# Kernel optimization log

Measured on AMD Instinct MI355X. Metric: run time of the kernel, lower is better.

The kernel has to match this reference:

```python
import jax, jax.numpy as jnp
import numpy as np

HID, H, LAT, R = 2048, 16, 512, 32
DH = HID // H          # 128 head_dim
C = DH - R             # 96 content_dim
B, S = 2, 2048


def rotate_half(x):
    h = x.shape[-1] // 2
    return jnp.concatenate([-x[..., h:], x[..., :h]], axis=-1)


def rope_tables(seq_len, dim):
    inv_freq = 1.0 / (10000.0 ** (jnp.arange(0, dim, 2, dtype=jnp.float32) / dim))
    t = jnp.arange(seq_len, dtype=jnp.float32)
    freqs = t[:, None] * inv_freq[None, :]          # [S, dim/2]
    emb = jnp.concatenate([freqs, freqs], axis=-1)  # [S, dim]
    return jnp.cos(emb), jnp.sin(emb)


def setup_inputs() -> dict:
    key = jax.random.key(0)
    ks = jax.random.split(key, 11)
    def lin(k, out_dim, in_dim):
        return jax.random.normal(k, (out_dim, in_dim), jnp.float32) / np.sqrt(in_dim)
    return {
        "x": jax.random.normal(ks[0], (B, S, HID), jnp.float32),
        "Wq_down": lin(ks[1], LAT, HID),
        "Wq_up": lin(ks[2], C * H, LAT),
        "Wq_rope": lin(ks[3], R * H, LAT),
        "Wkv_down": lin(ks[4], LAT, HID),
        "Wk_up": lin(ks[5], C * H, LAT),
        "Wk_rope": lin(ks[6], R, HID),
        "Wv_up": lin(ks[7], HID, LAT),
        "Wo": lin(ks[8], HID, HID),
        "bo": jnp.zeros((HID,), jnp.float32),
    }


def reference(x, Wq_down, Wq_up, Wq_rope, Wkv_down, Wk_up, Wk_rope, Wv_up, Wo, bo):
    Bs, Sl, _ = x.shape
    cos, sin = rope_tables(Sl, R)                       # [S, R]
    cos_b = cos[None, :, None, :]                       # [1,S,1,R]
    sin_b = sin[None, :, None, :]

    # low-rank Q path
    q_lat = jnp.einsum('bsh,lh->bsl', x, Wq_down)       # [B,S,LAT]
    q_c = jnp.einsum('bsl,cl->bsc', q_lat, Wq_up).reshape(Bs, Sl, H, C)
    q_r = jnp.einsum('bsl,rl->bsr', q_lat, Wq_rope).reshape(Bs, Sl, H, R)
    q_r = q_r * cos_b + rotate_half(q_r) * sin_b

    # low-rank KV path
    kv_lat = jnp.einsum('bsh,lh->bsl', x, Wkv_down)     # [B,S,LAT]
    k_c = jnp.einsum('bsl,cl->bsc', kv_lat, Wk_up).reshape(Bs, Sl, H, C)
    k_r = jnp.einsum('bsh,rh->bsr', x, Wk_rope)[:, :, None, :]   # [B,S,1,R]
    k_r = k_r * cos_b + rotate_half(k_r) * sin_b        # [B,S,1,R] (shared per head)
    k_r = jnp.broadcast_to(k_r, (Bs, Sl, H, R))
    v = jnp.einsum('bsl,dl->bsd', kv_lat, Wv_up).reshape(Bs, Sl, H, DH)

    q = jnp.concatenate([q_c, q_r], axis=-1)            # [B,S,H,DH]
    k = jnp.concatenate([k_c, k_r], axis=-1)

    scores = jnp.einsum('bqhd,bkhd->bhqk', q, k) / np.sqrt(DH)
    causal = jnp.triu(jnp.ones((Sl, Sl), bool), k=1)
    scores = jnp.where(causal[None, None], -10000.0, scores)
    attn = jax.nn.softmax(scores, axis=-1)
    ctx = jnp.einsum('bhqk,bkhd->bqhd', attn, v).reshape(Bs, Sl, HID)
    return jnp.einsum('bsd,od->bso', ctx, Wo) + bo
```

## Files before the change

### kernel.cpp

```cpp
#include <hip/hip_runtime.h>
#include <math.h>

#define HIDN 2048
#define NH   16
#define LATN 512
#define RD   32
#define DHD  128
#define CDIM 96
#define NB   2
#define SEQ  2048
#define MTOT 4096

typedef __attribute__((ext_vector_type(8))) short bf8_t;
typedef __attribute__((ext_vector_type(4))) float f4_t;
typedef __attribute__((ext_vector_type(4))) short s4_t;

__device__ __forceinline__ short f2bf(float f) {
    union { float f; unsigned u; } x; x.f = f;
    unsigned r = x.u + 0x7fffu + ((x.u >> 16) & 1u);
    return (short)(r >> 16);
}
__device__ __forceinline__ float bf2f(short s) {
    union { float f; unsigned u; } x; x.u = ((unsigned)(unsigned short)s) << 16;
    return x.f;
}
__device__ __forceinline__ void gload16(const void* g, void* l) {
    __builtin_amdgcn_global_load_lds(
        (const __attribute__((address_space(1))) void*)g,
        (__attribute__((address_space(3))) void*)l, 16, 0, 0);
}

__global__ __launch_bounds__(256)
void cvt_all(const float* __restrict__ x,  const float* __restrict__ w0,
             const float* __restrict__ w1, const float* __restrict__ w2,
             const float* __restrict__ w3, const float* __restrict__ w4,
             const float* __restrict__ w5, const float* __restrict__ w6,
             const float* __restrict__ w7,
             short* xb, short* o0, short* o1, short* o2, short* o3,
             short* o4, short* o5, short* o6, short* o7)
{
    int bid = blockIdx.x;
    const float* src; short* dst; int rel;
    if      (bid < 4096) { src = x;  dst = xb; rel = bid; }
    else if (bid < 4608) { src = w0; dst = o0; rel = bid - 4096; }
    else if (bid < 4992) { src = w1; dst = o1; rel = bid - 4608; }
    else if (bid < 5120) { src = w2; dst = o2; rel = bid - 4992; }
    else if (bid < 5632) { src = w3; dst = o3; rel = bid - 5120; }
    else if (bid < 6016) { src = w4; dst = o4; rel = bid - 5632; }
    else if (bid < 6048) { src = w5; dst = o5; rel = bid - 6016; }
    else if (bid < 6560) { src = w6; dst = o6; rel = bid - 6048; }
    else                 { src = w7; dst = o7; rel = bid - 6560; }
    int base = rel * 2048 + threadIdx.x * 8;
    float4 a = *(const float4*)(src + base);
    float4 b = *(const float4*)(src + base + 4);
    s4_t r0 = { f2bf(a.x), f2bf(a.y), f2bf(a.z), f2bf(a.w) };
    s4_t r1 = { f2bf(b.x), f2bf(b.y), f2bf(b.z), f2bf(b.w) };
    *(s4_t*)(dst + base)     = r0;
    *(s4_t*)(dst + base + 4) = r1;
}

#define EPI_DOWN 0
#define EPI_UP   1
#define EPI_WO   2

template<int KTOT, int EPI>
__global__ __launch_bounds__(256)
void gemm_t(const short* __restrict__ A, const short* __restrict__ W,
            const short* __restrict__ W2,
            void* __restrict__ o1, void* __restrict__ o2,
            void* __restrict__ o3, void* __restrict__ o4,
            const float* __restrict__ bias)
{
    __shared__ short As[2][4096];
    __shared__ short Bs[2][4096];
    const int tid  = threadIdx.x;
    const int w    = tid >> 6;
    const int lane = tid & 63;
    const int l16  = lane & 15;
    const int quad = lane >> 4;
    const int m0 = blockIdx.x * 128;
    int n0 = blockIdx.y * 128;
    const int wm = (w & 1) * 64;
    const int wn = (w >> 1) * 64;

    const short* Ap = A;
    const short* Wp = W;
    int lda, Nrow, job = 0;
    if (EPI == EPI_DOWN) { lda = 2048; Nrow = 1056; }
    if (EPI == EPI_WO)   { lda = 2048; Nrow = 2048; }
    if (EPI == EPI_UP) {
        lda = 1024;
        if (blockIdx.y < 16) { Nrow = 2048; }
        else { job = 1; Ap = A + 512; Wp = W2; n0 = ((int)blockIdx.y - 16) * 128; Nrow = 3584; }
    }

    int srow[2], skc[2], ldso[2];
#pragma unroll
    for (int j = 0; j < 2; ++j) {
        int c = (w * 32 + j * 16) * 4 + lane;
        srow[j] = c >> 2;
        skc[j]  = (c & 3) ^ (srow[j] & 3);
        ldso[j] = (w * 32 + j * 16) * 32;
    }
    const int xq = quad ^ (l16 & 3);

    auto stage = [&](int k0, int buf) {
#pragma unroll
        for (int j = 0; j < 2; ++j) {
            const short* ga = Ap + (size_t)(m0 + srow[j]) * lda + k0 + skc[j] * 8;
            gload16(ga, &As[buf][ldso[j]]);
            int gn = n0 + srow[j]; if (gn >= Nrow) gn = Nrow - 1;
            const short* gb = Wp + (size_t)gn * KTOT + k0 + skc[j] * 8;
            gload16(gb, &Bs[buf][ldso[j]]);
        }
    };

    f4_t acc[4][4];
#pragma unroll
    for (int i = 0; i < 4; ++i)
#pragma unroll
        for (int j = 0; j < 4; ++j) acc[i][j] = (f4_t){0.f, 0.f, 0.f, 0.f};

    stage(0, 0);
    const int nk = KTOT / 32;
    for (int t = 0; t < nk; ++t) {
        const int cur = t & 1;
        __syncthreads();
        if (t + 1 < nk) stage((t + 1) * 32, cur ^ 1);
        bf8_t af[4], bfr[4];
#pragma unroll
        for (int i = 0; i < 4; ++i)
            af[i] = *(const bf8_t*)&As[cur][((wm + i * 16 + l16) * 4 + xq) * 8];
#pragma unroll
        for (int j = 0; j < 4; ++j)
            bfr[j] = *(const bf8_t*)&Bs[cur][((wn + j * 16 + l16) * 4 + xq) * 8];
#pragma unroll
        for (int i = 0; i < 4; ++i)
#pragma unroll
            for (int j = 0; j < 4; ++j)
                acc[i][j] = __builtin_amdgcn_mfma_f32_16x16x32_bf16(
                    af[i], bfr[j], acc[i][j], 0, 0, 0);
    }

#pragma unroll
    for (int mi = 0; mi < 4; ++mi) {
#pragma unroll
        for (int nj = 0; nj < 4; ++nj) {
            const int gm = m0 + wm + mi * 16 + quad * 4;
            const int gn = n0 + wn + nj * 16 + l16;
            const int bb = gm >> 11, ss = gm & 2047;
            if (EPI == EPI_DOWN) {
                if (n0 < 1024) {
                    short* o = (short*)o1 + (size_t)gm * 1024 + gn;
#pragma unroll
                    for (int r = 0; r < 4; ++r) o[(size_t)r * 1024] = f2bf(acc[mi][nj][r]);
                } else if (gn < 1056) {
                    short* o = (short*)o2 + (size_t)gm * 32 + (gn - 1024);
#pragma unroll
                    for (int r = 0; r < 4; ++r) o[(size_t)r * 32] = f2bf(acc[mi][nj][r]);
                }
            } else if (EPI == EPI_WO) {
                float* o = (float*)o1 + (size_t)gm * 2048 + gn;
                float bv = bias[gn];
#pragma unroll
                for (int r = 0; r < 4; ++r) o[(size_t)r * 2048] = acc[mi][nj][r] + bv;
            } else {
                if (job == 0) {
                    if (gn < 1536) {
                        int hh = gn / CDIM, cc = gn % CDIM;
                        short* o = (short*)o1 +
                            (((size_t)(bb * NH + hh) * SEQ + ss) * DHD + cc);
#pragma unroll
                        for (int r = 0; r < 4; ++r) o[(size_t)r * DHD] = f2bf(acc[mi][nj][r]);
                    } else {
                        short* o = (short*)o2 + (size_t)gm * 512 + (gn - 1536);
#pragma unroll
                        for (int r = 0; r < 4; ++r) o[(size_t)r * 512] = f2bf(acc[mi][nj][r]);
                    }
                } else {
                    if (gn < 1536) {
                        int hh = gn / CDIM, cc = gn % CDIM;
                        short* o = (short*)o3 +
                            (((size_t)(bb * NH + hh) * SEQ + ss) * DHD + cc);
#pragma unroll
                        for (int r = 0; r < 4; ++r) o[(size_t)r * DHD] = f2bf(acc[mi][nj][r]);
                    } else {
                        int n2 = gn - 1536;
                        int h2 = n2 >> 7, dh = n2 & 127;
                        size_t idx = ((size_t)(bb * NH + h2) * DHD + dh) * SEQ + ss;
                        s4_t pk = { f2bf(acc[mi][nj][0]), f2bf(acc[mi][nj][1]),
                                    f2bf(acc[mi][nj][2]), f2bf(acc[mi][nj][3]) };
                        *(s4_t*)((short*)o4 + idx) = pk;
                    }
                }
            }
        }
    }
}

__global__ void rope_q_kernel(const short* __restrict__ qr, short* __restrict__ qh)
{
    int idx = blockIdx.x * blockDim.x + threadIdx.x;
    int m = idx >> 9;
    int h = (idx >> 5) & 15;
    int r = idx & 31;
    int b = m >> 11, s = m & (SEQ - 1);
    float invf = expf(-((float)(2 * (r & 15)) / 32.0f) * 9.210340371976184f);
    float f = (float)s * invf;
    float cs = cosf(f), sn = sinf(f);
    float val = bf2f(qr[(size_t)m * 512 + h * 32 + r]);
    float partner = bf2f(qr[(size_t)m * 512 + h * 32 + (r ^ 16)]);
    float rot = (r < 16) ? -partner : partner;
    qh[((size_t)(b * NH + h) * SEQ + s) * DHD + CDIM + r] = f2bf(val * cs + rot * sn);
}

__global__ void rope_k_kernel(const short* __restrict__ kr, short* __restrict__ kh)
{
    int idx = blockIdx.x * blockDim.x + threadIdx.x;
    int m = idx >> 5;
    int r = idx & 31;
    int b = m >> 11, s = m & (SEQ - 1);
    float invf = expf(-((float)(2 * (r & 15)) / 32.0f) * 9.210340371976184f);
    float f = (float)s * invf;
    float cs = cosf(f), sn = sinf(f);
    float val = bf2f(kr[(size_t)m * 32 + r]);
    float partner = bf2f(kr[(size_t)m * 32 + (r ^ 16)]);
    float rot = (r < 16) ? -partner : partner;
    short o = f2bf(val * cs + rot * sn);
    short* dst = kh + ((size_t)b * NH * SEQ + s) * DHD + CDIM + r;
#pragma unroll
    for (int h = 0; h < NH; ++h) dst[(size_t)h * SEQ * DHD] = o;
}

__global__ __launch_bounds__(256)
void attn_mfma(const short* __restrict__ qh, const short* __restrict__ kh,
               const short* __restrict__ vt, short* __restrict__ ctx)
{
    const int h = blockIdx.y, b = blockIdx.z;
    __shared__ short Ks[2][4096];
    __shared__ short Vs[2][4096];
    __shared__ short Ps[4][16][40];
    const int tid  = threadIdx.x;
    const int w    = tid >> 6;
    const int lane = tid & 63;
    const int l16  = lane & 15;
    const int quad = lane >> 4;
    const float scale = 0.08838834764831845f;

    const short* khead = kh + (size_t)(b * NH + h) * SEQ * DHD;
    const short* vhead = vt + (size_t)(b * NH + h) * DHD * SEQ;

    int koff[2], voff[2], ldso[2];
#pragma unroll
    for (int j = 0; j < 2; ++j) {
        int s = j * 256 + tid;
        int key = s >> 4, dch = (s & 15) ^ (key & 15);
        koff[j] = key * DHD + dch * 8;
        int d = s >> 2, kc = (s & 3) ^ ((d >> 1) & 3);
        voff[j] = d * SEQ + kc * 8;
        ldso[j] = (j * 256 + w * 64) * 8;
    }

    for (int phase = 0; phase < 2; ++phase) {
        const int qb = phase ? (31 - (int)blockIdx.x) : (int)blockIdx.x;
        const int q0 = qb * 64;

        bf8_t qf[4];
        {
            const short* qp = qh + ((size_t)(b * NH + h) * SEQ + q0 + w * 16 + l16) * DHD
                                 + quad * 8;
#pragma unroll
            for (int ks = 0; ks < 4; ++ks) {
                bf8_t raw = *(const bf8_t*)(qp + ks * 32);
#pragma unroll
                for (int j = 0; j < 8; ++j) qf[ks][j] = f2bf(bf2f(raw[j]) * scale);
            }
        }

        f4_t O[8];
#pragma unroll
        for (int i = 0; i < 8; ++i) O[i] = (f4_t){0.f, 0.f, 0.f, 0.f};
        float m_run[4], l_run[4];
#pragma unroll
        for (int r = 0; r < 4; ++r) { m_run[r] = -3e38f; l_run[r] = 0.f; }

        const int ntiles = 2 * qb + 2;
        __syncthreads();
#pragma unroll
        for (int j = 0; j < 2; ++j) {
            gload16(khead + koff[j], &Ks[0][ldso[j]]);
            gload16(vhead + voff[j], &Vs[0][ldso[j]]);
        }

        for (int t = 0; t < ntiles; ++t) {
            const int cur = t & 1;
            const int c0 = t * 32;
            __syncthreads();
            if (t + 1 < ntiles) {
                const short* kt = khead + (size_t)(c0 + 32) * DHD;
#pragma unroll
                for (int j = 0; j < 2; ++j) {
                    gload16(kt + koff[j], &Ks[cur ^ 1][ldso[j]]);
                    gload16(vhead + voff[j] + c0 + 32, &Vs[cur ^ 1][ldso[j]]);
                }
            }

            f4_t S0 = {0.f, 0.f, 0.f, 0.f}, S1 = {0.f, 0.f, 0.f, 0.f};
#pragma unroll
            for (int ks = 0; ks < 4; ++ks) {
                int dch = ks * 4 + quad;
                int si0 = l16 * 16 + (dch ^ l16);
                int si1 = (l16 + 16) * 16 + (dch ^ l16);
                bf8_t b0 = *(const bf8_t*)&Ks[cur][si0 * 8];
                bf8_t b1 = *(const bf8_t*)&Ks[cur][si1 * 8];
                S0 = __builtin_amdgcn_mfma_f32_16x16x32_bf16(qf[ks], b0, S0, 0, 0, 0);
                S1 = __builtin_amdgcn_mfma_f32_16x16x32_bf16(qf[ks], b1, S1, 0, 0, 0);
            }

            const int grow0 = q0 + w * 16 + quad * 4;
            float alpha[4];
#pragma unroll
            for (int r = 0; r < 4; ++r) {
                const int grow = grow0 + r;
                float s0 = (c0 + l16      <= grow) ? S0[r] : -3e38f;
                float s1 = (c0 + l16 + 16 <= grow) ? S1[r] : -3e38f;
                float mx = fmaxf(s0, s1);
                mx = fmaxf(mx, __shfl_xor(mx, 1));
                mx = fmaxf(mx, __shfl_xor(mx, 2));
                mx = fmaxf(mx, __shfl_xor(mx, 4));
                mx = fmaxf(mx, __shfl_xor(mx, 8));
                const float mnew = fmaxf(m_run[r], mx);
                alpha[r] = __expf(m_run[r] - mnew);
                const float p0 = __expf(s0 - mnew);
                const float p1 = __expf(s1 - mnew);
                float rs = p0 + p1;
                rs += __shfl_xor(rs, 1);
                rs += __shfl_xor(rs, 2);
                rs += __shfl_xor(rs, 4);
                rs += __shfl_xor(rs, 8);
                l_run[r] = alpha[r] * l_run[r] + rs;
                m_run[r] = mnew;
                Ps[w][quad * 4 + r][l16]      = f2bf(p0);
                Ps[w][quad * 4 + r][l16 + 16] = f2bf(p1);
            }

#pragma unroll
            for (int dt = 0; dt < 8; ++dt)
#pragma unroll
                for (int r = 0; r < 4; ++r) O[dt][r] *= alpha[r];

            bf8_t pf = *(const bf8_t*)&Ps[w][l16][quad * 8];
#pragma unroll
            for (int dt = 0; dt < 8; ++dt) {
                int d = dt * 16 + l16;
                int si = d * 4 + (quad ^ ((d >> 1) & 3));
                bf8_t vf = *(const bf8_t*)&Vs[cur][si * 8];
                O[dt] = __builtin_amdgcn_mfma_f32_16x16x32_bf16(pf, vf, O[dt], 0, 0, 0);
            }
        }

        float inv_l[4];
#pragma unroll
        for (int r = 0; r < 4; ++r) inv_l[r] = 1.0f / l_run[r];
        short* cbase = ctx + (size_t)(b * SEQ + q0 + w * 16 + quad * 4) * HIDN
                           + h * DHD + l16;
#pragma unroll
        for (int r = 0; r < 4; ++r)
#pragma unroll
            for (int dt = 0; dt < 8; ++dt)
                cbase[(size_t)r * HIDN + dt * 16] = f2bf(O[dt][r] * inv_l[r]);
    }
}

extern "C" void kernel_launch(void* const* d_in, const int* in_sizes, int n_in,
                              void* d_out, int out_size, void* d_ws, size_t ws_size,
                              hipStream_t stream)
{
    const float* x        = (const float*)d_in[0];
    const float* Wq_down  = (const float*)d_in[1];
    const float* Wq_up    = (const float*)d_in[2];
    const float* Wq_rope  = (const float*)d_in[3];
    const float* Wkv_down = (const float*)d_in[4];
    const float* Wk_up    = (const float*)d_in[5];
    const float* Wk_rope  = (const float*)d_in[6];
    const float* Wv_up    = (const float*)d_in[7];
    const float* Wo       = (const float*)d_in[8];
    const float* bo       = (const float*)d_in[9];
    float* out = (float*)d_out;

    short* ws     = (short*)d_ws;
    short* xb     = ws;
    short* wdownc = ws + 8388608;
    short* wqur   = ws + 10551296;
    short* wkvu   = ws + 11599872;
    short* wob    = ws + 13434880;
    short* qkvlat = ws + 17629184;
    short* qhb    = ws + 21823488;
    short* khb    = ws + 30212096;
    short* vtw    = ws + 38600704;
    short* ctxb   = ws + 46989312;
    short* qrt    = ws + 55377920;
    short* krt    = ws + 57475072;

    dim3 blk(256);
    cvt_all<<<dim3(8608), blk, 0, stream>>>(
        x, Wq_down, Wq_up, Wq_rope, Wkv_down, Wk_up, Wk_rope, Wv_up, Wo,
        xb, wdownc, wqur, wqur + 786432, wdownc + 1048576,
        wkvu, wdownc + 2097152, wkvu + 786432, wob);

    gemm_t<2048, EPI_DOWN><<<dim3(32, 9), blk, 0, stream>>>(
        xb, wdownc, nullptr, qkvlat, krt, nullptr, nullptr, nullptr);
    gemm_t<512, EPI_UP><<<dim3(32, 44), blk, 0, stream>>>(
        qkvlat, wqur, wkvu, qhb, qrt, khb, vtw, nullptr);

    rope_q_kernel<<<dim3(MTOT * NH * RD / 256), blk, 0, stream>>>(qrt, qhb);
    rope_k_kernel<<<dim3(MTOT * RD / 256), blk, 0, stream>>>(krt, khb);

    attn_mfma<<<dim3(16, NH, NB), blk, 0, stream>>>(qhb, khb, vtw, ctxb);

    gemm_t<2048, EPI_WO><<<dim3(32, 16), blk, 0, stream>>>(
        ctxb, wob, nullptr, out, nullptr, nullptr, nullptr, bo);
}
```

Before: 403.3 us.

## Widen attention key tile to 64, use DPP reductions and exp2 softmax

The flash-attention kernel now processes 64 keys per tile instead of 32, doubling the K/V LDS buffers and changing the V swizzle to an 8-chunk XOR pattern. This halves the number of tile iterations and barriers per query block. Row max and sum reductions switch from __shfl_xor to DPP row operations, and softmax uses exp2 with log2(e) folded into the query scale. The larger tiles raise LDS use to about 73 KB per block, which may lower occupancy.

```diff
diff --git a/kernel.cpp b/kernel.cpp
--- a/kernel.cpp
+++ b/kernel.cpp
@@ -28,6 +28,23 @@
     __builtin_amdgcn_global_load_lds(
         (const __attribute__((address_space(1))) void*)g,
         (__attribute__((address_space(3))) void*)l, 16, 0, 0);
+}
+
+__device__ __forceinline__ float dpp_max16(float x) {
+    union { float f; int i; } a, t; a.f = x;
+    t.i = __builtin_amdgcn_update_dpp(0, a.i, 0xB1,  0xF, 0xF, true); a.f = fmaxf(a.f, t.f);
+    t.i = __builtin_amdgcn_update_dpp(0, a.i, 0x4E,  0xF, 0xF, true); a.f = fmaxf(a.f, t.f);
+    t.i = __builtin_amdgcn_update_dpp(0, a.i, 0x124, 0xF, 0xF, true); a.f = fmaxf(a.f, t.f);
+    t.i = __builtin_amdgcn_update_dpp(0, a.i, 0x128, 0xF, 0xF, true); a.f = fmaxf(a.f, t.f);
+    return a.f;
+}
+__device__ __forceinline__ float dpp_sum16(float x) {
+    union { float f; int i; } a, t; a.f = x;
+    t.i = __builtin_amdgcn_update_dpp(0, a.i, 0xB1,  0xF, 0xF, true); a.f += t.f;
+    t.i = __builtin_amdgcn_update_dpp(0, a.i, 0x4E,  0xF, 0xF, true); a.f += t.f;
+    t.i = __builtin_amdgcn_update_dpp(0, a.i, 0x124, 0xF, 0xF, true); a.f += t.f;
+    t.i = __builtin_amdgcn_update_dpp(0, a.i, 0x128, 0xF, 0xF, true); a.f += t.f;
+    return a.f;
 }
 
 __global__ __launch_bounds__(256)
@@ -237,27 +254,27 @@
                const short* __restrict__ vt, short* __restrict__ ctx)
 {
     const int h = blockIdx.y, b = blockIdx.z;
-    __shared__ short Ks[2][4096];
-    __shared__ short Vs[2][4096];
-    __shared__ short Ps[4][16][40];
+    __shared__ short Ks[2][8192];
+    __shared__ short Vs[2][8192];
+    __shared__ short Ps[4][16][72];
     const int tid  = threadIdx.x;
     const int w    = tid >> 6;
     const int lane = tid & 63;
     const int l16  = lane & 15;
     const int quad = lane >> 4;
-    const float scale = 0.08838834764831845f;
+    const float qscale = 0.12752956f;
 
     const short* khead = kh + (size_t)(b * NH + h) * SEQ * DHD;
     const short* vhead = vt + (size_t)(b * NH + h) * DHD * SEQ;
 
-    int koff[2], voff[2], ldso[2];
-#pragma unroll
-    for (int j = 0; j < 2; ++j) {
+    int koff[4], voff[4], ldso[4];
+#pragma unroll
+    for (int j = 0; j < 4; ++j) {
         int s = j * 256 + tid;
-        int key = s >> 4, dch = (s & 15) ^ (key & 15);
-        koff[j] = key * DHD + dch * 8;
-        int d = s >> 2, kc = (s & 3) ^ ((d >> 1) & 3);
-        voff[j] = d * SEQ + kc * 8;
+        int key = s >> 4, c = s & 15;
+        koff[j] = key * DHD + (c ^ (key & 15)) * 8;
+        int d = s >> 3, c2 = s & 7;
+        voff[j] = d * SEQ + (c2 ^ (d & 7)) * 8;
         ldso[j] = (j * 256 + w * 64) * 8;
     }
 
@@ -273,7 +290,7 @@
             for (int ks = 0; ks < 4; ++ks) {
                 bf8_t raw = *(const bf8_t*)(qp + ks * 32);
 #pragma unroll
-                for (int j = 0; j < 8; ++j) qf[ks][j] = f2bf(bf2f(raw[j]) * scale);
+                for (int j = 0; j < 8; ++j) qf[ks][j] = f2bf(bf2f(raw[j]) * qscale);
             }
         }
 
@@ -284,37 +301,39 @@
 #pragma unroll
         for (int r = 0; r < 4; ++r) { m_run[r] = -3e38f; l_run[r] = 0.f; }
 
-        const int ntiles = 2 * qb + 2;
+        const int ntiles = qb + 1;
         __syncthreads();
 #pragma unroll
-        for (int j = 0; j < 2; ++j) {
+        for (int j = 0; j < 4; ++j) {
             gload16(khead + koff[j], &Ks[0][ldso[j]]);
             gload16(vhead + voff[j], &Vs[0][ldso[j]]);
         }
 
         for (int t = 0; t < ntiles; ++t) {
             const int cur = t & 1;
-            const int c0 = t * 32;
+            const int c0 = t * 64;
             __syncthreads();
             if (t + 1 < ntiles) {
-                const short* kt = khead + (size_t)(c0 + 32) * DHD;
-#pragma unroll
-                for (int j = 0; j < 2; ++j) {
+                const short* kt = khead + (size_t)(c0 + 64) * DHD;
+#pragma unroll
+                for (int j = 0; j < 4; ++j) {
                     gload16(kt + koff[j], &Ks[cur ^ 1][ldso[j]]);
-                    gload16(vhead + voff[j] + c0 + 32, &Vs[cur ^ 1][ldso[j]]);
+                    gload16(vhead + voff[j] + c0 + 64, &Vs[cur ^ 1][ldso[j]]);
                 }
             }
 
-            f4_t S0 = {0.f, 0.f, 0.f, 0.f}, S1 = {0.f, 0.f, 0.f, 0.f};
+            f4_t S[4];
+#pragma unroll
+            for (int j = 0; j < 4; ++j) S[j] = (f4_t){0.f, 0.f, 0.f, 0.f};
 #pragma unroll
             for (int ks = 0; ks < 4; ++ks) {
-                int dch = ks * 4 + quad;
-                int si0 = l16 * 16 + (dch ^ l16);
-                int si1 = (l16 + 16) * 16 + (dch ^ l16);
-                bf8_t b0 = *(const bf8_t*)&Ks[cur][si0 * 8];
-                bf8_t b1 = *(const bf8_t*)&Ks[cur][si1 * 8];
-                S0 = __builtin_amdgcn_mfma_f32_16x16x32_bf16(qf[ks], b0, S0, 0, 0, 0);
-                S1 = __builtin_amdgcn_mfma_f32_16x16x32_bf16(qf[ks], b1, S1, 0, 0, 0);
+                const int dch = ks * 4 + quad;
+#pragma unroll
+                for (int j = 0; j < 4; ++j) {
+                    const int slot = (j * 16 + l16) * 16 + (dch ^ l16);
+                    bf8_t bj = *(const bf8_t*)&Ks[cur][slot * 8];
+                    S[j] = __builtin_amdgcn_mfma_f32_16x16x32_bf16(qf[ks], bj, S[j], 0, 0, 0);
+                }
             }
 
             const int grow0 = q0 + w * 16 + quad * 4;
@@ -322,26 +341,26 @@
 #pragma unroll
             for (int r = 0; r < 4; ++r) {
                 const int grow = grow0 + r;
-                float s0 = (c0 + l16      <= grow) ? S0[r] : -3e38f;
-                float s1 = (c0 + l16 + 16 <= grow) ? S1[r] : -3e38f;
-                float mx = fmaxf(s0, s1);
-                mx = fmaxf(mx, __shfl_xor(mx, 1));
-                mx = fmaxf(mx, __shfl_xor(mx, 2));
-                mx = fmaxf(mx, __shfl_xor(mx, 4));
-                mx = fmaxf(mx, __shfl_xor(mx, 8));
+                float sv[4];
+#pragma unroll
+                for (int j = 0; j < 4; ++j)
+                    sv[j] = (c0 + j * 16 + l16 <= grow) ? S[j][r] : -3e38f;
+                float mx = fmaxf(fmaxf(sv[0], sv[1]), fmaxf(sv[2], sv[3]));
+                mx = dpp_max16(mx);
                 const float mnew = fmaxf(m_run[r], mx);
-                alpha[r] = __expf(m_run[r] - mnew);
-                const float p0 = __expf(s0 - mnew);
-                const float p1 = __expf(s1 - mnew);
-                float rs = p0 + p1;
-                rs += __shfl_xor(rs, 1);
-                rs += __shfl_xor(rs, 2);
-                rs += __shfl_xor(rs, 4);
-                rs += __shfl_xor(rs, 8);
+                alpha[r] = __builtin_amdgcn_exp2f(m_run[r] - mnew);
+                float p0 = __builtin_amdgcn_exp2f(sv[0] - mnew);
+                float p1 = __builtin_amdgcn_exp2f(sv[1] - mnew);
+                float p2 = __builtin_amdgcn_exp2f(sv[2] - mnew);
+                float p3 = __builtin_amdgcn_exp2f(sv[3] - mnew);
+                float rs = dpp_sum16((p0 + p1) + (p2 + p3));
                 l_run[r] = alpha[r] * l_run[r] + rs;
                 m_run[r] = mnew;
-                Ps[w][quad * 4 + r][l16]      = f2bf(p0);
-                Ps[w][quad * 4 + r][l16 + 16] = f2bf(p1);
+                short* pr = &Ps[w][quad * 4 + r][l16];
+                pr[0]  = f2bf(p0);
+                pr[16] = f2bf(p1);
+                pr[32] = f2bf(p2);
+                pr[48] = f2bf(p3);
             }
 
 #pragma unroll
@@ -349,13 +368,16 @@
 #pragma unroll
                 for (int r = 0; r < 4; ++r) O[dt][r] *= alpha[r];
 
-            bf8_t pf = *(const bf8_t*)&Ps[w][l16][quad * 8];
-#pragma unroll
-            for (int dt = 0; dt < 8; ++dt) {
-                int d = dt * 16 + l16;
-                int si = d * 4 + (quad ^ ((d >> 1) & 3));
-                bf8_t vf = *(const bf8_t*)&Vs[cur][si * 8];
-                O[dt] = __builtin_amdgcn_mfma_f32_16x16x32_bf16(pf, vf, O[dt], 0, 0, 0);
+#pragma unroll
+            for (int ks2 = 0; ks2 < 2; ++ks2) {
+                bf8_t pf = *(const bf8_t*)&Ps[w][l16][ks2 * 32 + quad * 8];
+#pragma unroll
+                for (int dt = 0; dt < 8; ++dt) {
+                    const int d = dt * 16 + l16;
+                    const int slot = d * 8 + ((ks2 * 4 + quad) ^ (d & 7));
+                    bf8_t vf = *(const bf8_t*)&Vs[cur][slot * 8];
+                    O[dt] = __builtin_amdgcn_mfma_f32_16x16x32_bf16(pf, vf, O[dt], 0, 0, 0);
+                }
             }
         }
 
```

Result: faster. 355.2 us (-11.9%).
